# Optimization experiments

Measured on AMD Instinct MI355X. Metric: run time of the kernel, lower is better.

Reference implementation:

```python
import jax, jax.numpy as jnp
import numpy as np

N_STORE, N_DEPT, F_IN = 100_000, 20_000, 128
E = 1_000_000
H, C = 4, 16  # heads, per-head channels; hidden = H*C = 64
NUM_LAYERS = 3


def setup_inputs() -> dict:
    key = jax.random.key(0)
    ks = jax.random.split(key, 16)
    def edges(k, n_src, n_dst):
        k1, k2 = jax.random.split(k)
        src = jax.random.randint(k1, (E,), 0, n_src, dtype=jnp.int32)
        dst = jax.random.randint(k2, (E,), 0, n_dst, dtype=jnp.int32)
        return jnp.stack([src, dst])
    s = 0.05
    return {
        "x_store": jax.random.normal(ks[0], (N_STORE, F_IN), jnp.float32),
        "x_dept": jax.random.normal(ks[1], (N_DEPT, F_IN), jnp.float32),
        "edge_sd": edges(ks[2], N_STORE, N_DEPT),   # store -> dept
        "edge_ds": edges(ks[3], N_DEPT, N_STORE),   # dept  -> store
        "edge_ss": edges(ks[4], N_STORE, N_STORE),  # store -> store
        "W_src0": jax.random.normal(ks[5], (3, F_IN, H * C), jnp.float32) * s,
        "W_dst0": jax.random.normal(ks[6], (3, F_IN, H * C), jnp.float32) * s,
        "W_src_h": jax.random.normal(ks[7], (2, 3, H * C, H * C), jnp.float32) * s,
        "W_dst_h": jax.random.normal(ks[8], (2, 3, H * C, H * C), jnp.float32) * s,
        "att_src": jax.random.normal(ks[9], (3, 3, H, C), jnp.float32) * s,
        "att_dst": jax.random.normal(ks[10], (3, 3, H, C), jnp.float32) * s,
        "bias": jnp.zeros((3, 3, H * C), jnp.float32),
    }


def gat_conv(x_src, x_dst, edge, W_s, W_d, a_s, a_d, b, n_dst):
    """PyG GATConv, bipartite, add_self_loops=False, eval mode (no dropout)."""
    h_s = (x_src @ W_s).reshape(-1, H, C)   # [N_src, H, C]
    h_d = (x_dst @ W_d).reshape(-1, H, C)   # [N_dst, H, C]
    al_s = jnp.sum(h_s * a_s, axis=-1)      # [N_src, H]
    al_d = jnp.sum(h_d * a_d, axis=-1)      # [N_dst, H]
    src, dst = edge[0], edge[1]
    e = jax.nn.leaky_relu(al_s[src] + al_d[dst], 0.2)        # [E, H]
    m = jax.ops.segment_max(e, dst, num_segments=n_dst)       # segment softmax
    m = jnp.where(jnp.isfinite(m), m, 0.0)
    ex = jnp.exp(e - m[dst])
    denom = jax.ops.segment_sum(ex, dst, num_segments=n_dst)
    alpha = ex / (denom[dst] + 1e-16)                          # [E, H]
    msg = h_s[src] * alpha[:, :, None]                         # [E, H, C]
    out = jax.ops.segment_sum(msg, dst, num_segments=n_dst)    # [N_dst, H, C]
    return out.reshape(n_dst, H * C) + b


def _forward(x_store, x_dept, edge_sd, edge_ds, edge_ss,
             W_src0, W_dst0, W_src_h, W_dst_h, att_src, att_dst, bias):
    xs, xd = x_store, x_dept
    for i in range(NUM_LAYERS):
        Ws = W_src0 if i == 0 else W_src_h[i - 1]
        Wd = W_dst0 if i == 0 else W_dst_h[i - 1]
        # edge type 0: store->dept ; 1: dept->store ; 2: store->store
        o_dept = gat_conv(xs, xd, edge_sd, Ws[0], Wd[0], att_src[i, 0], att_dst[i, 0], bias[i, 0], N_DEPT)
        o1 = gat_conv(xd, xs, edge_ds, Ws[1], Wd[1], att_src[i, 1], att_dst[i, 1], bias[i, 1], N_STORE)
        o2 = gat_conv(xs, xs, edge_ss, Ws[2], Wd[2], att_src[i, 2], att_dst[i, 2], bias[i, 2], N_STORE)
        o_store = (o1 + o2) * 0.5  # HeteroConv aggr='mean' across relations into 'store'
        if i < NUM_LAYERS - 1:
            xs, xd = jax.nn.relu(o_store), jax.nn.relu(o_dept)  # dropout is identity in eval
        else:
            xs, xd = o_store, o_dept
    return jnp.concatenate([xs, xd], axis=0)  # [N_STORE + N_DEPT, 64]


def reference(x_store, x_dept, edge_sd, edge_ds, edge_ss,
              W_src0, W_dst0, W_src_h, W_dst_h, att_src, att_dst, bias):
    return _forward(x_store, x_dept, edge_sd, edge_ds, edge_ss,
                    W_src0, W_dst0, W_src_h, W_dst_h, att_src, att_dst, bias)
```

## Files before the change

kernel.cpp:

```cpp
#include <hip/hip_runtime.h>
#include <hip/hip_bf16.h>

#define N_STORE 100000
#define N_DEPT  20000
#define F_IN    128
#define NTOT    (N_DEPT + 2 * N_STORE)

#define NB0   157
#define NB12  196
#define NBUCK (NB0 + 2 * NB12)

using u16    = unsigned short;
using bf16x8 = __attribute__((ext_vector_type(8))) __bf16;
using f32x4  = __attribute__((ext_vector_type(4))) float;

__device__ __forceinline__ float b2f(u16 x) {
    unsigned u = ((unsigned)x) << 16;
    return __builtin_bit_cast(float, u);
}
__device__ __forceinline__ u16 f2b(float f) {
    unsigned u = __builtin_bit_cast(unsigned, f);
    u += 0x7FFFu + ((u >> 16) & 1u);
    return (u16)(u >> 16);
}

__global__ void k_zeroi(int* p, int n) {
    int i = blockIdx.x * 256 + threadIdx.x;
    if (i < n) p[i] = 0;
}

__global__ void k_bcount(const int* __restrict__ e0, const int* __restrict__ e1,
                         const int* __restrict__ e2, int E, int* __restrict__ bucketCnt) {
    __shared__ int c[256];
    int t = threadIdx.x;
    c[t] = 0; __syncthreads();
    int rel = blockIdx.y;
    const int* e = (rel == 0) ? e0 : (rel == 1) ? e1 : e2;
    int n = (rel == 0) ? N_DEPT : N_STORE;
    int shift = (rel == 0) ? 7 : 9;
    int i0 = blockIdx.x * 2048 + t;
#pragma unroll
    for (int k = 0; k < 8; ++k) {
        int i = i0 + k * 256;
        if (i < E) {
            int d = e[E + i];
            if ((unsigned)d < (unsigned)n) atomicAdd(&c[d >> shift], 1);
        }
    }
    __syncthreads();
    int bbase = (rel == 0) ? 0 : (rel == 1) ? NB0 : NB0 + NB12;
    int nb = (rel == 0) ? NB0 : NB12;
    if (t < nb && c[t]) atomicAdd(&bucketCnt[bbase + t], c[t]);
}

__global__ void k_bscan(const int* __restrict__ bucketCnt, int* __restrict__ bucketOfs,
                        int* __restrict__ bucketCur, int* __restrict__ offs) {
    __shared__ int s[1024];
    int t = threadIdx.x;
    int v = (t < NBUCK) ? bucketCnt[t] : 0;
    s[t] = v; __syncthreads();
    for (int o = 1; o < 1024; o <<= 1) {
        int u = (t >= o) ? s[t - o] : 0;
        __syncthreads();
        s[t] += u;
        __syncthreads();
    }
    if (t < NBUCK) {
        bucketOfs[t + 1] = s[t];
        bucketCur[t] = s[t] - v;
    }
    if (t == 0) bucketOfs[0] = 0;
    if (t == NBUCK - 1) offs[NTOT] = s[t];
}

__global__ void k_bscatter(const int* __restrict__ e0, const int* __restrict__ e1,
                           const int* __restrict__ e2, int E,
                           int* __restrict__ bucketCur, unsigned* __restrict__ pairs) {
    __shared__ int c[256];
    __shared__ int base[256];
    int t = threadIdx.x;
    c[t] = 0; __syncthreads();
    int rel = blockIdx.y;
    const int* e = (rel == 0) ? e0 : (rel == 1) ? e1 : e2;
    int n = (rel == 0) ? N_DEPT : N_STORE;
    int shift = (rel == 0) ? 7 : 9;
    int i0 = blockIdx.x * 2048 + t;
    int mb[8], mr[8]; unsigned mv[8];
#pragma unroll
    for (int k = 0; k < 8; ++k) {
        int i = i0 + k * 256;
        mb[k] = -1;
        if (i < E) {
            int d = e[E + i];
            if ((unsigned)d < (unsigned)n) {
                int b = d >> shift;
                mb[k] = b;
                mr[k] = atomicAdd(&c[b], 1);
                mv[k] = (unsigned)e[i] | ((unsigned)(d - (b << shift)) << 20);
            }
        }
    }
    __syncthreads();
    int bbase = (rel == 0) ? 0 : (rel == 1) ? NB0 : NB0 + NB12;
    int nb = (rel == 0) ? NB0 : NB12;
    if (t < nb && c[t]) base[t] = atomicAdd(&bucketCur[bbase + t], c[t]);
    __syncthreads();
#pragma unroll
    for (int k = 0; k < 8; ++k)
        if (mb[k] >= 0) pairs[base[mb[k]] + mr[k]] = mv[k];
}

__global__ void k_bfinal(const unsigned* __restrict__ pairs, const int* __restrict__ bucketOfs,
                         int* __restrict__ offs, int* __restrict__ srcs_all) {
    int b = blockIdx.x, t = threadIdx.x;
    int rel = (b < NB0) ? 0 : (b < NB0 + NB12) ? 1 : 2;
    int shift = (rel == 0) ? 7 : 9;
    int bLocal = b - ((rel == 0) ? 0 : (rel == 1) ? NB0 : NB0 + NB12);
    int n = (rel == 0) ? N_DEPT : N_STORE;
    int gbase = (rel == 0) ? 0 : (rel == 1) ? N_DEPT : N_DEPT + N_STORE;
    int nodeLo = bLocal << shift;
    int bsize = 1 << shift;
    int nNodes = n - nodeLo; if (nNodes > bsize) nNodes = bsize;
    int pairLo = bucketOfs[b], pairHi = bucketOfs[b + 1];
    __shared__ int cnt[512], sc[512];
    cnt[t] = 0; cnt[t + 256] = 0;
    __syncthreads();
    for (int p = pairLo + t; p < pairHi; p += 256)
        atomicAdd(&cnt[pairs[p] >> 20], 1);
    __syncthreads();
    sc[t] = cnt[t]; sc[t + 256] = cnt[t + 256];
    __syncthreads();
    for (int o = 1; o < 512; o <<= 1) {
        int a0 = (t >= o) ? sc[t - o] : 0;
        int a1 = (t + 256 >= o) ? sc[t + 256 - o] : 0;
        __syncthreads();
        sc[t] += a0; sc[t + 256] += a1;
        __syncthreads();
    }
    int ex0 = sc[t] - cnt[t];
    int ex1 = sc[t + 256] - cnt[t + 256];
    if (t < nNodes)       offs[gbase + nodeLo + t]       = pairLo + ex0;
    if (t + 256 < nNodes) offs[gbase + nodeLo + t + 256] = pairLo + ex1;
    __syncthreads();
    cnt[t] = ex0; cnt[t + 256] = ex1;
    __syncthreads();
    for (int p = pairLo + t; p < pairHi; p += 256) {
        unsigned u = pairs[p];
        int q = atomicAdd(&cnt[u >> 20], 1);
        srcs_all[pairLo + q] = (int)(u & 0xFFFFFu);
    }
}

__global__ void k_pack_store(const float* __restrict__ Wa, const float* __restrict__ Wb,
                             const float* __restrict__ Wd1, const float* __restrict__ Wd2,
                             const float* __restrict__ aS0, const float* __restrict__ aS2,
                             const float* __restrict__ aD1, const float* __restrict__ aD2,
                             int K, u16* __restrict__ out) {
    int id = blockIdx.x * 256 + threadIdx.x;
    int total = K * 144;
    if (id >= total) return;
    int k = id / 144, n = id - k * 144;
    float val;
    if (n < 64) val = Wa[k * 64 + n];
    else if (n < 128) val = Wb[k * 64 + (n - 64)];
    else {
        int g = (n - 128) >> 2, h = (n - 128) & 3;
        const float* W = (g == 0) ? Wa : (g == 1) ? Wb : (g == 2) ? Wd1 : Wd2;
        const float* a = (g == 0) ? aS0 : (g == 1) ? aS2 : (g == 2) ? aD1 : aD2;
        float acc = 0.f;
        for (int c = 0; c < 16; ++c) acc += W[k * 64 + h * 16 + c] * a[h * 16 + c];
        val = acc;
    }
    int KT = K >> 5;
    int ct = n >> 4, col = n & 15, kt = k >> 5, q = (k >> 3) & 3, j = k & 7;
    out[(size_t)((ct * KT + kt) * 64 + q * 16 + col) * 8 + j] = f2b(val);
}

__global__ void k_pack_dept(const float* __restrict__ Ws1, const float* __restrict__ Wd0,
                            const float* __restrict__ aD0, const float* __restrict__ aS1,
                            int K, u16* __restrict__ out) {
    int id = blockIdx.x * 256 + threadIdx.x;
    int total = K * 80;
    if (id >= total) return;
    int k = id / 80, n = id - k * 80;
    float val;
    if (n < 64) val = Ws1[k * 64 + n];
    else if (n < 72) {
        int g = (n - 64) >> 2, h = (n - 64) & 3;
        const float* W = g ? Ws1 : Wd0;
        const float* a = g ? aS1 : aD0;
        float acc = 0.f;
        for (int c = 0; c < 16; ++c) acc += W[k * 64 + h * 16 + c] * a[h * 16 + c];
        val = acc;
    } else val = 0.f;
    int KT = K >> 5;
    int ct = n >> 4, col = n & 15, kt = k >> 5, q = (k >> 3) & 3, j = k & 7;
    out[(size_t)((ct * KT + kt) * 64 + q * 16 + col) * 8 + j] = f2b(val);
}

template <int KT, int CVT, int MODE>
__global__ void k_gemm(const void* __restrict__ Ain, int nrows, int K,
                       const u16* __restrict__ Bpanel,
                       u16* __restrict__ H0, u16* __restrict__ H1, u16* __restrict__ AL) {
    const int CT = (MODE == 0) ? 9 : 5;
    int wid = (blockIdx.x * blockDim.x + threadIdx.x) >> 6;
    int lane = threadIdx.x & 63;
    int m0 = wid << 4;
    if (m0 >= nrows) return;
    int r = lane & 15, q = lane >> 4;
    bf16x8 a[KT];
    if (CVT) {
        const float* ap = (const float*)Ain + (size_t)(m0 + r) * K + q * 8;
#pragma unroll
        for (int kt = 0; kt < KT; ++kt) {
            f32x4 f0 = *(const f32x4*)(ap + kt * 32);
            f32x4 f1 = *(const f32x4*)(ap + kt * 32 + 4);
            bf16x8 v;
#pragma unroll
            for (int j = 0; j < 4; ++j) {
                v[j]     = __builtin_bit_cast(__bf16, f2b(f0[j]));
                v[4 + j] = __builtin_bit_cast(__bf16, f2b(f1[j]));
            }
            a[kt] = v;
        }
    } else {
        const u16* ap = (const u16*)Ain + (size_t)(m0 + r) * K + q * 8;
#pragma unroll
        for (int kt = 0; kt < KT; ++kt) a[kt] = *(const bf16x8*)(ap + kt * 32);
    }
    const bf16x8* B = (const bf16x8*)Bpanel;
    int rowb = m0 + q * 4;
#pragma unroll
    for (int ct = 0; ct < CT; ++ct) {
        f32x4 acc = {0.f, 0.f, 0.f, 0.f};
#pragma unroll
        for (int kt = 0; kt < KT; ++kt)
            acc = __builtin_amdgcn_mfma_f32_16x16x32_bf16(a[kt], B[(ct * KT + kt) * 64 + lane], acc, 0, 0, 0);
        if (MODE == 0) {
            if (ct < 4) {
                u16* cp = H0 + (size_t)rowb * 64 + ct * 16 + r;
#pragma unroll
                for (int i = 0; i < 4; ++i) cp[(size_t)i * 64] = f2b(acc[i]);
            } else if (ct < 8) {
                u16* cp = H1 + (size_t)rowb * 64 + (ct - 4) * 16 + r;
#pragma unroll
                for (int i = 0; i < 4; ++i) cp[(size_t)i * 64] = f2b(acc[i]);
            } else {
                u16* cp = AL + (size_t)rowb * 16 + r;
#pragma unroll
                for (int i = 0; i < 4; ++i) cp[(size_t)i * 16] = f2b(acc[i]);
            }
        } else {
            if (ct < 4) {
                u16* cp = H0 + (size_t)rowb * 64 + ct * 16 + r;
#pragma unroll
                for (int i = 0; i < 4; ++i) cp[(size_t)i * 64] = f2b(acc[i]);
            } else {
                u16* cp = AL + (size_t)rowb * 16 + r;
#pragma unroll
                for (int i = 0; i < 4; ++i) cp[(size_t)i * 16] = f2b(acc[i]);
            }
        }
    }
}

__device__ __forceinline__ float warp16_sum(float v) {
    v += __shfl_xor(v, 1);
    v += __shfl_xor(v, 2);
    v += __shfl_xor(v, 4);
    v += __shfl_xor(v, 8);
    return v;
}

__device__ __forceinline__ void agg_seg(const int* __restrict__ srcs, int j0, int j1, int nsrc,
                                        const u16* __restrict__ htab, const u16* __restrict__ altab,
                                        int alsOff, int lane, int slot, int h, int pbase, float ald,
                                        float& acc, float& den) {
    for (int j = j0; j < j1; j += 16) {
        int nb = j1 - j; if (nb > 16) nb = 16;
        int sv = srcs[j + (slot < nb ? slot : 0)];
        sv = ((unsigned)sv < (unsigned)nsrc) ? sv : 0;
        u16 avr = altab[(size_t)sv * 16 + alsOff + h];
        float hv[16];
#pragma unroll
        for (int k = 0; k < 16; ++k) {
            int s = __builtin_amdgcn_readlane(sv, k);
            hv[k] = b2f(htab[(size_t)s * 64 + lane]);
        }
        float e = b2f(avr) + ald;
        e = (e > 0.f) ? e : 0.2f * e;
        float ex = (slot < nb) ? __expf(e) : 0.f;
        den += ex;
        int exi = __builtin_bit_cast(int, ex);
#pragma unroll
        for (int k = 0; k < 16; ++k) {
            float exv = __builtin_bit_cast(float,
                __builtin_amdgcn_ds_bpermute(pbase + (k << 2), exi));
            acc = fmaf(exv, hv[k], acc);
        }
    }
}

__global__ void k_agg1(const int* __restrict__ offs, const int* __restrict__ srcs,
                       const u16* __restrict__ hS0, const u16* __restrict__ alS,
                       const u16* __restrict__ alD,
                       const float* __restrict__ bias, int doRelu,
                       u16* __restrict__ bOut, float* __restrict__ fOut) {
    int wid = (blockIdx.x * blockDim.x + threadIdx.x) >> 6;
    if (wid >= N_DEPT) return;
    int lane = threadIdx.x & 63, slot = lane & 15, h = lane >> 4;
    int pbase = (lane & 48) << 2;
    float ald = b2f(alD[(size_t)wid * 16 + 0 + h]);
    int j0 = __builtin_amdgcn_readfirstlane(offs[wid]);
    int j1 = __builtin_amdgcn_readfirstlane(offs[wid + 1]);
    float acc = 0.f, den = 0.f;
    agg_seg(srcs, j0, j1, N_STORE, hS0, alS, 0, lane, slot, h, pbase, ald, acc, den);
    den = warp16_sum(den);
    float out = acc / (den + 1e-16f) + bias[lane];
    if (doRelu) out = out > 0.f ? out : 0.f;
    size_t oi = (size_t)wid * 64 + lane;
    if (fOut) fOut[oi] = out;
    else      bOut[oi] = f2b(out);
}

__global__ void k_agg2(const int* __restrict__ offs1, const int* __restrict__ srcs,
                       const int* __restrict__ offs2,
                       const u16* __restrict__ hD, const u16* __restrict__ alD,
                       const u16* __restrict__ hS2, const u16* __restrict__ alS,
                       const float* __restrict__ bias1, const float* __restrict__ bias2,
                       int doRelu,
                       u16* __restrict__ bOut, float* __restrict__ fOut) {
    int wid = (blockIdx.x * blockDim.x + threadIdx.x) >> 6;
    if (wid >= N_STORE) return;
    int lane = threadIdx.x & 63, slot = lane & 15, h = lane >> 4;
    int pbase = (lane & 48) << 2;
    float ald1 = b2f(alS[(size_t)wid * 16 + 8 + h]);
    float ald2 = b2f(alS[(size_t)wid * 16 + 12 + h]);
    int a0 = __builtin_amdgcn_readfirstlane(offs1[wid]);
    int a1e = __builtin_amdgcn_readfirstlane(offs1[wid + 1]);
    int b0 = __builtin_amdgcn_readfirstlane(offs2[wid]);
    int b1e = __builtin_amdgcn_readfirstlane(offs2[wid + 1]);
    float acc1 = 0.f, den1 = 0.f, acc2 = 0.f, den2 = 0.f;
    agg_seg(srcs, a0, a1e, N_DEPT, hD, alD, 4, lane, slot, h, pbase, ald1, acc1, den1);
    agg_seg(srcs, b0, b1e, N_STORE, hS2, alS, 4, lane, slot, h, pbase, ald2, acc2, den2);
    den1 = warp16_sum(den1);
    den2 = warp16_sum(den2);
    float out = (acc1 / (den1 + 1e-16f) + bias1[lane] + acc2 / (den2 + 1e-16f) + bias2[lane]) * 0.5f;
    if (doRelu) out = out > 0.f ? out : 0.f;
    size_t oi = (size_t)wid * 64 + lane;
    if (fOut) fOut[oi] = out;
    else      bOut[oi] = f2b(out);
}

extern "C" void kernel_launch(void* const* d_in, const int* in_sizes, int n_in,
                              void* d_out, int out_size, void* d_ws, size_t ws_size,
                              hipStream_t stream) {
    const float* x_store = (const float*)d_in[0];
    const float* x_dept  = (const float*)d_in[1];
    const int* e_sd = (const int*)d_in[2];
    const int* e_ds = (const int*)d_in[3];
    const int* e_ss = (const int*)d_in[4];
    const float* W_src0  = (const float*)d_in[5];
    const float* W_dst0  = (const float*)d_in[6];
    const float* W_src_h = (const float*)d_in[7];
    const float* W_dst_h = (const float*)d_in[8];
    const float* att_src = (const float*)d_in[9];
    const float* att_dst = (const float*)d_in[10];
    const float* bias    = (const float*)d_in[11];
    const int E = in_sizes[2] / 2;

    char* w = (char*)d_ws;
    auto alloc = [&](size_t bytes) -> char* {
        char* p = w;
        w += (bytes + 255) & ~(size_t)255;
        return p;
    };
    int* offs_all  = (int*)alloc((size_t)(NTOT + 1) * 4);
    int* srcs_all  = (int*)alloc((size_t)3 * E * 4);
    int* bucketCnt = (int*)alloc(1024 * 4);
    int* bucketOfs = (int*)alloc(1024 * 4);
    int* bucketCur = (int*)alloc(1024 * 4);
    u16* panelS[3]; u16* panelD[3];
    for (int l = 0; l < 3; ++l) {
        int KT = (l == 0) ? 4 : 2;
        panelS[l] = (u16*)alloc((size_t)KT * 9 * 64 * 8 * 2);
        panelD[l] = (u16*)alloc((size_t)KT * 5 * 64 * 8 * 2);
    }
    u16* hS0   = (u16*)alloc((size_t)N_STORE * 64 * 2);
    u16* hS2   = (u16*)alloc((size_t)N_STORE * 64 * 2);
    u16* alS   = (u16*)alloc((size_t)N_STORE * 16 * 2);
    u16* hD    = (u16*)alloc((size_t)N_DEPT * 64 * 2);
    u16* alD   = (u16*)alloc((size_t)N_DEPT * 16 * 2);
    u16* actSA = (u16*)alloc((size_t)N_STORE * 64 * 2);
    u16* actDA = (u16*)alloc((size_t)N_DEPT * 64 * 2);
    u16* actSB = actSA;
    u16* actDB = actDA;
    unsigned* pairs = (unsigned*)hS0;

    int* off_sd = offs_all;
    int* off_ds = offs_all + N_DEPT;
    int* off_ss = offs_all + N_DEPT + N_STORE;

    float* outStoreF = (float*)d_out;
    float* outDeptF  = outStoreF + (size_t)N_STORE * 64;

    int ebl8 = (E + 2047) / 2048;
    k_zeroi<<<(NBUCK + 255) / 256, 256, 0, stream>>>(bucketCnt, NBUCK);
    k_bcount<<<dim3(ebl8, 3), 256, 0, stream>>>(e_sd, e_ds, e_ss, E, bucketCnt);
    k_bscan<<<1, 1024, 0, stream>>>(bucketCnt, bucketOfs, bucketCur, offs_all);
    k_bscatter<<<dim3(ebl8, 3), 256, 0, stream>>>(e_sd, e_ds, e_ss, E, bucketCur, pairs);
    k_bfinal<<<NBUCK, 256, 0, stream>>>(pairs, bucketOfs, offs_all, srcs_all);

    for (int l = 0; l < 3; ++l) {
        int K = (l == 0) ? 128 : 64;
        const float *Ws[3], *Wd[3], *aS[3], *aD[3];
        for (int rr = 0; rr < 3; ++rr) {
            Ws[rr] = (l == 0) ? W_src0 + (size_t)rr * 128 * 64
                              : W_src_h + (size_t)((l - 1) * 3 + rr) * 64 * 64;
            Wd[rr] = (l == 0) ? W_dst0 + (size_t)rr * 128 * 64
                              : W_dst_h + (size_t)((l - 1) * 3 + rr) * 64 * 64;
            aS[rr] = att_src + (size_t)(l * 3 + rr) * 64;
            aD[rr] = att_dst + (size_t)(l * 3 + rr) * 64;
        }
        k_pack_store<<<(K * 144 + 255) / 256, 256, 0, stream>>>(
            Ws[0], Ws[2], Wd[1], Wd[2], aS[0], aS[2], aD[1], aD[2], K, panelS[l]);
        k_pack_dept<<<(K * 80 + 255) / 256, 256, 0, stream>>>(
            Ws[1], Wd[0], aD[0], aS[1], K, panelD[l]);

        int gbS = (N_STORE / 16 * 64 + 255) / 256;
        int gbD = (N_DEPT / 16 * 64 + 255) / 256;
        if (l == 0) {
            k_gemm<4, 1, 0><<<gbS, 256, 0, stream>>>(x_store, N_STORE, K, panelS[l], hS0, hS2, alS);
            k_gemm<4, 1, 1><<<gbD, 256, 0, stream>>>(x_dept, N_DEPT, K, panelD[l], hD, nullptr, alD);
        } else if (l == 1) {
            k_gemm<2, 0, 0><<<gbS, 256, 0, stream>>>(actSA, N_STORE, K, panelS[l], hS0, hS2, alS);
            k_gemm<2, 0, 1><<<gbD, 256, 0, stream>>>(actDA, N_DEPT, K, panelD[l], hD, nullptr, alD);
        } else {
            k_gemm<2, 0, 0><<<gbS, 256, 0, stream>>>(actSB, N_STORE, K, panelS[l], hS0, hS2, alS);
            k_gemm<2, 0, 1><<<gbD, 256, 0, stream>>>(actDB, N_DEPT, K, panelD[l], hD, nullptr, alD);
        }

        int relu = (l < 2) ? 1 : 0;
        u16* bS = (l == 0) ? actSA : actSB;
        u16* bD = (l == 0) ? actDA : actDB;
        float* fS = (l == 2) ? outStoreF : nullptr;
        float* fD = (l == 2) ? outDeptF  : nullptr;
        k_agg1<<<N_DEPT / 4, 256, 0, stream>>>(
            off_sd, srcs_all, hS0, alS, alD,
            bias + (size_t)(l * 3 + 0) * 64, relu, bD, fD);
        k_agg2<<<N_STORE / 4, 256, 0, stream>>>(
            off_ds, srcs_all, off_ss,
            hD, alD, hS2, alS,
            bias + (size_t)(l * 3 + 1) * 64, bias + (size_t)(l * 3 + 2) * 64,
            relu, bS, fS);
    }
    (void)n_in; (void)out_size; (void)ws_size;
}
```

Baseline: 578.5 us.

## Split dept aggregation across two waves and interleave store relations' gathers

k_agg1 now assigns two wavefronts per dept node, each handling half of the incoming edge list in 16-edge chunks, and combines partial numerators and denominators through shared memory. This targets the high in-degree of dept nodes (about 50 edges each), which left few long-running waves. k_agg2 fuses the two per-relation edge loops into a single loop that issues both relations' gathers before consuming them, aiming for more memory-level parallelism. The cost is a block barrier and LDS traffic in k_agg1, and higher register use in k_agg2 from two 16-element gather buffers.

New measurement: 650.2 us. 12.4% more time.

```diff
diff --git a/kernel.cpp b/kernel.cpp
--- a/kernel.cpp
+++ b/kernel.cpp
@@ -301,26 +301,45 @@
     }
 }
 
-__global__ void k_agg1(const int* __restrict__ offs, const int* __restrict__ srcs,
+__global__ void __launch_bounds__(256) k_agg1(
+                       const int* __restrict__ offs, const int* __restrict__ srcs,
                        const u16* __restrict__ hS0, const u16* __restrict__ alS,
                        const u16* __restrict__ alD,
                        const float* __restrict__ bias, int doRelu,
                        u16* __restrict__ bOut, float* __restrict__ fOut) {
-    int wid = (blockIdx.x * blockDim.x + threadIdx.x) >> 6;
-    if (wid >= N_DEPT) return;
+    __shared__ float sAcc[4][64];
+    __shared__ float sDen[4][64];
+    int wl = threadIdx.x >> 6;
+    int gwid = (blockIdx.x * blockDim.x + threadIdx.x) >> 6;
+    int node = gwid >> 1, half = gwid & 1;
     int lane = threadIdx.x & 63, slot = lane & 15, h = lane >> 4;
     int pbase = (lane & 48) << 2;
-    float ald = b2f(alD[(size_t)wid * 16 + 0 + h]);
-    int j0 = __builtin_amdgcn_readfirstlane(offs[wid]);
-    int j1 = __builtin_amdgcn_readfirstlane(offs[wid + 1]);
     float acc = 0.f, den = 0.f;
-    agg_seg(srcs, j0, j1, N_STORE, hS0, alS, 0, lane, slot, h, pbase, ald, acc, den);
-    den = warp16_sum(den);
-    float out = acc / (den + 1e-16f) + bias[lane];
-    if (doRelu) out = out > 0.f ? out : 0.f;
-    size_t oi = (size_t)wid * 64 + lane;
-    if (fOut) fOut[oi] = out;
-    else      bOut[oi] = f2b(out);
+    bool active = node < N_DEPT;
+    if (active) {
+        float ald = b2f(alD[(size_t)node * 16 + 0 + h]);
+        int j0 = __builtin_amdgcn_readfirstlane(offs[node]);
+        int j1 = __builtin_amdgcn_readfirstlane(offs[node + 1]);
+        int cnt = j1 - j0;
+        int mid = j0 + (((cnt + 31) >> 5) << 4);
+        if (mid > j1) mid = j1;
+        int s = half ? mid : j0;
+        int e = half ? j1 : mid;
+        agg_seg(srcs, s, e, N_STORE, hS0, alS, 0, lane, slot, h, pbase, ald, acc, den);
+        den = warp16_sum(den);
+    }
+    sAcc[wl][lane] = acc;
+    sDen[wl][lane] = den;
+    __syncthreads();
+    if (active && half == 0) {
+        float accT = acc + sAcc[wl + 1][lane];
+        float denT = den + sDen[wl + 1][lane];
+        float out = accT / (denT + 1e-16f) + bias[lane];
+        if (doRelu) out = out > 0.f ? out : 0.f;
+        size_t oi = (size_t)node * 64 + lane;
+        if (fOut) fOut[oi] = out;
+        else      bOut[oi] = f2b(out);
+    }
 }
 
 __global__ void k_agg2(const int* __restrict__ offs1, const int* __restrict__ srcs,
@@ -336,13 +355,74 @@
     int pbase = (lane & 48) << 2;
     float ald1 = b2f(alS[(size_t)wid * 16 + 8 + h]);
     float ald2 = b2f(alS[(size_t)wid * 16 + 12 + h]);
-    int a0 = __builtin_amdgcn_readfirstlane(offs1[wid]);
-    int a1e = __builtin_amdgcn_readfirstlane(offs1[wid + 1]);
-    int b0 = __builtin_amdgcn_readfirstlane(offs2[wid]);
-    int b1e = __builtin_amdgcn_readfirstlane(offs2[wid + 1]);
+    int ja = __builtin_amdgcn_readfirstlane(offs1[wid]);
+    int a1 = __builtin_amdgcn_readfirstlane(offs1[wid + 1]);
+    int jb = __builtin_amdgcn_readfirstlane(offs2[wid]);
+    int b1 = __builtin_amdgcn_readfirstlane(offs2[wid + 1]);
     float acc1 = 0.f, den1 = 0.f, acc2 = 0.f, den2 = 0.f;
-    agg_seg(srcs, a0, a1e, N_DEPT, hD, alD, 4, lane, slot, h, pbase, ald1, acc1, den1);
-    agg_seg(srcs, b0, b1e, N_STORE, hS2, alS, 4, lane, slot, h, pbase, ald2, acc2, den2);
+    while (ja < a1 || jb < b1) {
+        int nb1 = a1 - ja; nb1 = nb1 > 16 ? 16 : nb1;
+        int nb2 = b1 - jb; nb2 = nb2 > 16 ? 16 : nb2;
+        int sv1 = 0, sv2 = 0;
+        u16 av1 = 0, av2 = 0;
+        if (nb1 > 0) {
+            int v = srcs[ja + (slot < nb1 ? slot : 0)];
+            sv1 = ((unsigned)v < (unsigned)N_DEPT) ? v : 0;
+            av1 = alD[(size_t)sv1 * 16 + 4 + h];
+        }
+        if (nb2 > 0) {
+            int v = srcs[jb + (slot < nb2 ? slot : 0)];
+            sv2 = ((unsigned)v < (unsigned)N_STORE) ? v : 0;
+            av2 = alS[(size_t)sv2 * 16 + 4 + h];
+        }
+        u16 hv1[16], hv2[16];
+        if (nb1 > 0) {
+#pragma unroll
+            for (int k = 0; k < 16; ++k) {
+                int s = __builtin_amdgcn_readlane(sv1, k);
+                hv1[k] = hD[(size_t)s * 64 + lane];
+            }
+        }
+        if (nb2 > 0) {
+#pragma unroll
+            for (int k = 0; k < 16; ++k) {
+                int s = __builtin_amdgcn_readlane(sv2, k);
+                hv2[k] = hS2[(size_t)s * 64 + lane];
+            }
+        }
+        int exi1 = 0, exi2 = 0;
+        if (nb1 > 0) {
+            float e = b2f(av1) + ald1;
+            e = (e > 0.f) ? e : 0.2f * e;
+            float ex = (slot < nb1) ? __expf(e) : 0.f;
+            den1 += ex;
+            exi1 = __builtin_bit_cast(int, ex);
+        }
+        if (nb2 > 0) {
+            float e = b2f(av2) + ald2;
+            e = (e > 0.f) ? e : 0.2f * e;
+            float ex = (slot < nb2) ? __expf(e) : 0.f;
+            den2 += ex;
+            exi2 = __builtin_bit_cast(int, ex);
+        }
+        if (nb1 > 0) {
+#pragma unroll
+            for (int k = 0; k < 16; ++k) {
+                float exv = __builtin_bit_cast(float,
+                    __builtin_amdgcn_ds_bpermute(pbase + (k << 2), exi1));
+                acc1 = fmaf(exv, b2f(hv1[k]), acc1);
+            }
+        }
+        if (nb2 > 0) {
+#pragma unroll
+            for (int k = 0; k < 16; ++k) {
+                float exv = __builtin_bit_cast(float,
+                    __builtin_amdgcn_ds_bpermute(pbase + (k << 2), exi2));
+                acc2 = fmaf(exv, b2f(hv2[k]), acc2);
+            }
+        }
+        ja += 16; jb += 16;
+    }
     den1 = warp16_sum(den1);
     den2 = warp16_sum(den2);
     float out = (acc1 / (den1 + 1e-16f) + bias1[lane] + acc2 / (den2 + 1e-16f) + bias2[lane]) * 0.5f;
@@ -445,7 +525,7 @@
         u16* bD = (l == 0) ? actDA : actDB;
         float* fS = (l == 2) ? outStoreF : nullptr;
         float* fD = (l == 2) ? outDeptF  : nullptr;
-        k_agg1<<<N_DEPT / 4, 256, 0, stream>>>(
+        k_agg1<<<N_DEPT / 2, 256, 0, stream>>>(
             off_sd, srcs_all, hS0, alS, alD,
             bias + (size_t)(l * 3 + 0) * 64, relu, bD, fD);
         k_agg2<<<N_STORE / 4, 256, 0, stream>>>(
```

## Split attention logits into compact per-relation tables and halve dept aggregation per wave

Applied to the files above, without the earlier changes.

The GEMM epilogue now writes the attention logits into separate compact tables with 4 or 8 values per node, replacing one interleaved 16-wide table. Gathered source logits then touch fewer bytes and cache lines per edge. The dept aggregation kernel splits each node's edge list across two waves and combines the partial sums through shared memory. Dept nodes average about 50 incoming edges, so this adds parallelism and shortens the serial chain per wave, at the cost of a block-wide sync and more launched waves.

New measurement: 566.2 us. 1.02x faster.

```diff
diff --git a/kernel.cpp b/kernel.cpp
--- a/kernel.cpp
+++ b/kernel.cpp
@@ -201,7 +201,8 @@
 template <int KT, int CVT, int MODE>
 __global__ void k_gemm(const void* __restrict__ Ain, int nrows, int K,
                        const u16* __restrict__ Bpanel,
-                       u16* __restrict__ H0, u16* __restrict__ H1, u16* __restrict__ AL) {
+                       u16* __restrict__ H0, u16* __restrict__ H1,
+                       u16* __restrict__ A0, u16* __restrict__ A1, u16* __restrict__ A2) {
     const int CT = (MODE == 0) ? 9 : 5;
     int wid = (blockIdx.x * blockDim.x + threadIdx.x) >> 6;
     int lane = threadIdx.x & 63;
@@ -236,29 +237,27 @@
 #pragma unroll
         for (int kt = 0; kt < KT; ++kt)
             acc = __builtin_amdgcn_mfma_f32_16x16x32_bf16(a[kt], B[(ct * KT + kt) * 64 + lane], acc, 0, 0, 0);
-        if (MODE == 0) {
-            if (ct < 4) {
-                u16* cp = H0 + (size_t)rowb * 64 + ct * 16 + r;
-#pragma unroll
-                for (int i = 0; i < 4; ++i) cp[(size_t)i * 64] = f2b(acc[i]);
-            } else if (ct < 8) {
-                u16* cp = H1 + (size_t)rowb * 64 + (ct - 4) * 16 + r;
-#pragma unroll
-                for (int i = 0; i < 4; ++i) cp[(size_t)i * 64] = f2b(acc[i]);
-            } else {
-                u16* cp = AL + (size_t)rowb * 16 + r;
-#pragma unroll
-                for (int i = 0; i < 4; ++i) cp[(size_t)i * 16] = f2b(acc[i]);
-            }
+        if (ct < 4) {
+            u16* cp = H0 + (size_t)rowb * 64 + ct * 16 + r;
+#pragma unroll
+            for (int i = 0; i < 4; ++i) cp[(size_t)i * 64] = f2b(acc[i]);
+        } else if (MODE == 0 && ct < 8) {
+            u16* cp = H1 + (size_t)rowb * 64 + (ct - 4) * 16 + r;
+#pragma unroll
+            for (int i = 0; i < 4; ++i) cp[(size_t)i * 64] = f2b(acc[i]);
         } else {
-            if (ct < 4) {
-                u16* cp = H0 + (size_t)rowb * 64 + ct * 16 + r;
-#pragma unroll
-                for (int i = 0; i < 4; ++i) cp[(size_t)i * 64] = f2b(acc[i]);
-            } else {
-                u16* cp = AL + (size_t)rowb * 16 + r;
-#pragma unroll
-                for (int i = 0; i < 4; ++i) cp[(size_t)i * 16] = f2b(acc[i]);
+            if (r < 4) {
+                u16* cp = A0 + (size_t)rowb * 4 + r;
+#pragma unroll
+                for (int i = 0; i < 4; ++i) cp[(size_t)i * 4] = f2b(acc[i]);
+            } else if (r < 8) {
+                u16* cp = A1 + (size_t)rowb * 4 + (r - 4);
+#pragma unroll
+                for (int i = 0; i < 4; ++i) cp[(size_t)i * 4] = f2b(acc[i]);
+            } else if (MODE == 0) {
+                u16* cp = A2 + (size_t)rowb * 8 + (r - 8);
+#pragma unroll
+                for (int i = 0; i < 4; ++i) cp[(size_t)i * 8] = f2b(acc[i]);
             }
         }
     }
@@ -274,13 +273,13 @@
 
 __device__ __forceinline__ void agg_seg(const int* __restrict__ srcs, int j0, int j1, int nsrc,
                                         const u16* __restrict__ htab, const u16* __restrict__ altab,
-                                        int alsOff, int lane, int slot, int h, int pbase, float ald,
+                                        int lane, int slot, int h, int pbase, float ald,
                                         float& acc, float& den) {
     for (int j = j0; j < j1; j += 16) {
         int nb = j1 - j; if (nb > 16) nb = 16;
         int sv = srcs[j + (slot < nb ? slot : 0)];
         sv = ((unsigned)sv < (unsigned)nsrc) ? sv : 0;
-        u16 avr = altab[(size_t)sv * 16 + alsOff + h];
+        u16 avr = altab[(size_t)sv * 4 + h];
         float hv[16];
 #pragma unroll
         for (int k = 0; k < 16; ++k) {
@@ -301,32 +300,52 @@
     }
 }
 
-__global__ void k_agg1(const int* __restrict__ offs, const int* __restrict__ srcs,
-                       const u16* __restrict__ hS0, const u16* __restrict__ alS,
-                       const u16* __restrict__ alD,
+__global__ void __launch_bounds__(256) k_agg1(
+                       const int* __restrict__ offs, const int* __restrict__ srcs,
+                       const u16* __restrict__ hS0, const u16* __restrict__ alsS0,
+                       const u16* __restrict__ aldD0,
                        const float* __restrict__ bias, int doRelu,
                        u16* __restrict__ bOut, float* __restrict__ fOut) {
-    int wid = (blockIdx.x * blockDim.x + threadIdx.x) >> 6;
-    if (wid >= N_DEPT) return;
+    __shared__ float sAcc[4][64];
+    __shared__ float sDen[4][64];
+    int wl = threadIdx.x >> 6;
+    int gwid = (blockIdx.x * blockDim.x + threadIdx.x) >> 6;
+    int node = gwid >> 1, half = gwid & 1;
     int lane = threadIdx.x & 63, slot = lane & 15, h = lane >> 4;
     int pbase = (lane & 48) << 2;
-    float ald = b2f(alD[(size_t)wid * 16 + 0 + h]);
-    int j0 = __builtin_amdgcn_readfirstlane(offs[wid]);
-    int j1 = __builtin_amdgcn_readfirstlane(offs[wid + 1]);
     float acc = 0.f, den = 0.f;
-    agg_seg(srcs, j0, j1, N_STORE, hS0, alS, 0, lane, slot, h, pbase, ald, acc, den);
-    den = warp16_sum(den);
-    float out = acc / (den + 1e-16f) + bias[lane];
-    if (doRelu) out = out > 0.f ? out : 0.f;
-    size_t oi = (size_t)wid * 64 + lane;
-    if (fOut) fOut[oi] = out;
-    else      bOut[oi] = f2b(out);
+    bool active = node < N_DEPT;
+    if (active) {
+        float ald = b2f(aldD0[(size_t)node * 4 + h]);
+        int j0 = __builtin_amdgcn_readfirstlane(offs[node]);
+        int j1 = __builtin_amdgcn_readfirstlane(offs[node + 1]);
+        int cnt = j1 - j0;
+        int mid = j0 + (((cnt + 31) >> 5) << 4);
+        if (mid > j1) mid = j1;
+        int s = half ? mid : j0;
+        int e = half ? j1 : mid;
+        agg_seg(srcs, s, e, N_STORE, hS0, alsS0, lane, slot, h, pbase, ald, acc, den);
+        den = warp16_sum(den);
+    }
+    sAcc[wl][lane] = acc;
+    sDen[wl][lane] = den;
+    __syncthreads();
+    if (active && half == 0) {
+        float accT = acc + sAcc[wl + 1][lane];
+        float denT = den + sDen[wl + 1][lane];
+        float out = accT / (denT + 1e-16f) + bias[lane];
+        if (doRelu) out = out > 0.f ? out : 0.f;
+        size_t oi = (size_t)node * 64 + lane;
+        if (fOut) fOut[oi] = out;
+        else      bOut[oi] = f2b(out);
+    }
 }
 
 __global__ void k_agg2(const int* __restrict__ offs1, const int* __restrict__ srcs,
                        const int* __restrict__ offs2,
-                       const u16* __restrict__ hD, const u16* __restrict__ alD,
-                       const u16* __restrict__ hS2, const u16* __restrict__ alS,
+                       const u16* __restrict__ hD, const u16* __restrict__ alsD1,
+                       const u16* __restrict__ hS2, const u16* __restrict__ alsS2,
+                       const u16* __restrict__ aldS12,
                        const float* __restrict__ bias1, const float* __restrict__ bias2,
                        int doRelu,
                        u16* __restrict__ bOut, float* __restrict__ fOut) {
@@ -334,15 +353,15 @@
     if (wid >= N_STORE) return;
     int lane = threadIdx.x & 63, slot = lane & 15, h = lane >> 4;
     int pbase = (lane & 48) << 2;
-    float ald1 = b2f(alS[(size_t)wid * 16 + 8 + h]);
-    float ald2 = b2f(alS[(size_t)wid * 16 + 12 + h]);
+    float ald1 = b2f(aldS12[(size_t)wid * 8 + h]);
+    float ald2 = b2f(aldS12[(size_t)wid * 8 + 4 + h]);
     int a0 = __builtin_amdgcn_readfirstlane(offs1[wid]);
     int a1e = __builtin_amdgcn_readfirstlane(offs1[wid + 1]);
     int b0 = __builtin_amdgcn_readfirstlane(offs2[wid]);
     int b1e = __builtin_amdgcn_readfirstlane(offs2[wid + 1]);
     float acc1 = 0.f, den1 = 0.f, acc2 = 0.f, den2 = 0.f;
-    agg_seg(srcs, a0, a1e, N_DEPT, hD, alD, 4, lane, slot, h, pbase, ald1, acc1, den1);
-    agg_seg(srcs, b0, b1e, N_STORE, hS2, alS, 4, lane, slot, h, pbase, ald2, acc2, den2);
+    agg_seg(srcs, a0, a1e, N_DEPT, hD, alsD1, lane, slot, h, pbase, ald1, acc1, den1);
+    agg_seg(srcs, b0, b1e, N_STORE, hS2, alsS2, lane, slot, h, pbase, ald2, acc2, den2);
     den1 = warp16_sum(den1);
     den2 = warp16_sum(den2);
     float out = (acc1 / (den1 + 1e-16f) + bias1[lane] + acc2 / (den2 + 1e-16f) + bias2[lane]) * 0.5f;
@@ -386,15 +405,18 @@
         panelS[l] = (u16*)alloc((size_t)KT * 9 * 64 * 8 * 2);
         panelD[l] = (u16*)alloc((size_t)KT * 5 * 64 * 8 * 2);
     }
-    u16* hS0   = (u16*)alloc((size_t)N_STORE * 64 * 2);
-    u16* hS2   = (u16*)alloc((size_t)N_STORE * 64 * 2);
-    u16* alS   = (u16*)alloc((size_t)N_STORE * 16 * 2);
-    u16* hD    = (u16*)alloc((size_t)N_DEPT * 64 * 2);
-    u16* alD   = (u16*)alloc((size_t)N_DEPT * 16 * 2);
-    u16* actSA = (u16*)alloc((size_t)N_STORE * 64 * 2);
-    u16* actDA = (u16*)alloc((size_t)N_DEPT * 64 * 2);
-    u16* actSB = actSA;
-    u16* actDB = actDA;
+    u16* hS0    = (u16*)alloc((size_t)N_STORE * 64 * 2);
+    u16* hS2    = (u16*)alloc((size_t)N_STORE * 64 * 2);
+    u16* hD     = (u16*)alloc((size_t)N_DEPT * 64 * 2);
+    u16* alsS0  = (u16*)alloc((size_t)N_STORE * 4 * 2);
+    u16* alsS2  = (u16*)alloc((size_t)N_STORE * 4 * 2);
+    u16* aldS12 = (u16*)alloc((size_t)N_STORE * 8 * 2);
+    u16* aldD0  = (u16*)alloc((size_t)N_DEPT * 4 * 2);
+    u16* alsD1  = (u16*)alloc((size_t)N_DEPT * 4 * 2);
+    u16* actSA  = (u16*)alloc((size_t)N_STORE * 64 * 2);
+    u16* actDA  = (u16*)alloc((size_t)N_DEPT * 64 * 2);
+    u16* actSB  = actSA;
+    u16* actDB  = actDA;
     unsigned* pairs = (unsigned*)hS0;
 
     int* off_sd = offs_all;
@@ -430,14 +452,20 @@
         int gbS = (N_STORE / 16 * 64 + 255) / 256;
         int gbD = (N_DEPT / 16 * 64 + 255) / 256;
         if (l == 0) {
-            k_gemm<4, 1, 0><<<gbS, 256, 0, stream>>>(x_store, N_STORE, K, panelS[l], hS0, hS2, alS);
-            k_gemm<4, 1, 1><<<gbD, 256, 0, stream>>>(x_dept, N_DEPT, K, panelD[l], hD, nullptr, alD);
+            k_gemm<4, 1, 0><<<gbS, 256, 0, stream>>>(x_store, N_STORE, K, panelS[l],
+                                                     hS0, hS2, alsS0, alsS2, aldS12);
+            k_gemm<4, 1, 1><<<gbD, 256, 0, stream>>>(x_dept, N_DEPT, K, panelD[l],
+                                                     hD, nullptr, aldD0, alsD1, nullptr);
         } else if (l == 1) {
-            k_gemm<2, 0, 0><<<gbS, 256, 0, stream>>>(actSA, N_STORE, K, panelS[l], hS0, hS2, alS);
-            k_gemm<2, 0, 1><<<gbD, 256, 0, stream>>>(actDA, N_DEPT, K, panelD[l], hD, nullptr, alD);
+            k_gemm<2, 0, 0><<<gbS, 256, 0, stream>>>(actSA, N_STORE, K, panelS[l],
+                                                     hS0, hS2, alsS0, alsS2, aldS12);
+            k_gemm<2, 0, 1><<<gbD, 256, 0, stream>>>(actDA, N_DEPT, K, panelD[l],
+                                                     hD, nullptr, aldD0, alsD1, nullptr);
         } else {
-            k_gemm<2, 0, 0><<<gbS, 256, 0, stream>>>(actSB, N_STORE, K, panelS[l], hS0, hS2, alS);
-            k_gemm<2, 0, 1><<<gbD, 256, 0, stream>>>(actDB, N_DEPT, K, panelD[l], hD, nullptr, alD);
+            k_gemm<2, 0, 0><<<gbS, 256, 0, stream>>>(actSB, N_STORE, K, panelS[l],
+                                                     hS0, hS2, alsS0, alsS2, aldS12);
+            k_gemm<2, 0, 1><<<gbD, 256, 0, stream>>>(actDB, N_DEPT, K, panelD[l],
+                                                     hD, nullptr, aldD0, alsD1, nullptr);
         }
 
         int relu = (l < 2) ? 1 : 0;
@@ -445,12 +473,12 @@
         u16* bD = (l == 0) ? actDA : actDB;
         float* fS = (l == 2) ? outStoreF : nullptr;
         float* fD = (l == 2) ? outDeptF  : nullptr;
-        k_agg1<<<N_DEPT / 4, 256, 0, stream>>>(
-            off_sd, srcs_all, hS0, alS, alD,
+        k_agg1<<<N_DEPT / 2, 256, 0, stream>>>(
+            off_sd, srcs_all, hS0, alsS0, aldD0,
             bias + (size_t)(l * 3 + 0) * 64, relu, bD, fD);
         k_agg2<<<N_STORE / 4, 256, 0, stream>>>(
             off_ds, srcs_all, off_ss,
-            hD, alD, hS2, alS,
+            hD, alsD1, hS2, alsS2, aldS12,
             bias + (size_t)(l * 3 + 1) * 64, bias + (size_t)(l * 3 + 2) * 64,
             relu, bS, fS);
     }
```
